# Kernel optimization log

Hardware: AMD Instinct MI355X
Metric: run time of the kernel (lower is better)

The kernel has to match this reference:

```python
import jax, jax.numpy as jnp
import numpy as np

# Model dims (match init_kwargs)
D_MODEL = 512
NUM_EXPERTS = 8
TOP_K = 2
FFN_MULT = 2
HIDDEN = FFN_MULT * D_MODEL
BATCH, SEQ = 4, 2048


def setup_inputs() -> dict:
    key = jax.random.key(0)
    k_x, k_g, k_bg, k_w1, k_w3, k_w2 = jax.random.split(key, 6)
    sd = 1.0 / np.sqrt(D_MODEL).astype(np.float32)
    sh = 1.0 / np.sqrt(HIDDEN).astype(np.float32)
    return {
        "x": jax.random.normal(k_x, (BATCH, SEQ, D_MODEL), dtype=jnp.float32),
        # gate: nn.Linear(d_model, num_experts) with bias
        "Wg": jax.random.normal(k_g, (D_MODEL, NUM_EXPERTS), dtype=jnp.float32) * sd,
        "bg": jax.random.normal(k_bg, (NUM_EXPERTS,), dtype=jnp.float32) * 0.01,
        # stacked per-expert SwiGLU FFN params (no bias, LLaMA-style)
        "W1": jax.random.normal(k_w1, (NUM_EXPERTS, D_MODEL, HIDDEN), dtype=jnp.float32) * sd,
        "W3": jax.random.normal(k_w3, (NUM_EXPERTS, D_MODEL, HIDDEN), dtype=jnp.float32) * sd,
        "W2": jax.random.normal(k_w2, (NUM_EXPERTS, HIDDEN, D_MODEL), dtype=jnp.float32) * sh,
    }


def reference(x, Wg, bg, W1, W3, W2):
    B, S, D = x.shape
    E = Wg.shape[1]
    xt = x.reshape(-1, D)                        # [T, D], T = B*S
    T = xt.shape[0]

    # Router: top-k over experts, softmax over the k selected logits
    logits = xt @ Wg + bg                        # [T, E]
    top_vals, top_idx = jax.lax.top_k(logits, TOP_K)  # [T, K]
    top_probs = jax.nn.softmax(top_vals, axis=-1)     # [T, K]

    # Dense per-(token, expert) combine weight; zero where expert not selected.
    # top-k indices are distinct per token so scatter-add == scatter-set.
    gate_w = jnp.zeros((T, E), dtype=xt.dtype).at[
        jnp.arange(T)[:, None], top_idx
    ].add(top_probs)                              # [T, E]

    # Loop over experts (fixed, small), accumulate weighted expert outputs.
    def body(y, expert):
        w1, w3, w2, g = expert                   # g: [T]
        h = jax.nn.silu(xt @ w1) * (xt @ w3)     # [T, H]
        return y + g[:, None] * (h @ w2), None

    y0 = jnp.zeros_like(xt)
    y, _ = jax.lax.scan(body, y0, (W1, W3, W2, gate_w.T))
    return y.reshape(B, S, D)
```

## Files before the change

kernel.cpp:

```cpp
#include <hip/hip_runtime.h>
#include <hip/hip_bf16.h>

#define TOKENS 8192
#define DM 512
#define NE 8
#define HID 1024
#define NSLOT (TOKENS * 2)
#define NB 32

#define BM 128
#define BN 64
#define BK 64
#define MAXTILE 136

typedef __bf16 bf16x8 __attribute__((ext_vector_type(8)));
typedef float floatx4 __attribute__((ext_vector_type(4)));
typedef unsigned short u16x8 __attribute__((ext_vector_type(8)));

__device__ __forceinline__ unsigned short f2bf(float f) {
    union { float f; unsigned u; } c; c.f = f;
    unsigned u = c.u;
    u += 0x7fffu + ((u >> 16) & 1u);
    return (unsigned short)(u >> 16);
}

__device__ __forceinline__ void load16_lds(const void* g, void* l) {
    __builtin_amdgcn_global_load_lds(
        (const __attribute__((address_space(1))) unsigned int*)g,
        (__attribute__((address_space(3))) unsigned int*)l, 16, 0, 0);
}

__global__ void cvt_transpose_kernel(const float* __restrict__ W1, const float* __restrict__ W3,
                                     const float* __restrict__ W2,
                                     unsigned short* __restrict__ w1t, unsigned short* __restrict__ w3t,
                                     unsigned short* __restrict__ w2t) {
    __shared__ float tile[64][65];
    const float* src; unsigned short* dst; int K, N;
    if (blockIdx.y == 0)      { src = W1; dst = w1t; K = DM;  N = HID; }
    else if (blockIdx.y == 1) { src = W3; dst = w3t; K = DM;  N = HID; }
    else                      { src = W2; dst = w2t; K = HID; N = DM;  }
    const int tkn = (K >> 6) * (N >> 6);
    int b = blockIdx.x;
    int e = b / tkn;
    int rem = b % tkn;
    const int tn6 = N >> 6;
    int kt = rem / tn6, nt = rem % tn6;
    int tx = threadIdx.x & 15, ty = threadIdx.x >> 4;
    const float* s = src + ((size_t)(e * K + kt * 64 + ty)) * N + nt * 64 + tx * 4;
    #pragma unroll
    for (int i = 0; i < 4; i++) {
        float4 v = *(const float4*)(s + (size_t)(i * 16) * N);
        float* tr = &tile[ty + i * 16][tx * 4];
        tr[0] = v.x; tr[1] = v.y; tr[2] = v.z; tr[3] = v.w;
    }
    __syncthreads();
    int n = threadIdx.x >> 3;
    int c8 = (threadIdx.x & 7) * 8;
    unsigned short* d = dst + ((size_t)(e * N + nt * 64)) * K + kt * 64;
    #pragma unroll
    for (int i = 0; i < 2; i++) {
        int nn = n + i * 32;
        u16x8 r;
        #pragma unroll
        for (int kk = 0; kk < 8; kk++) r[kk] = f2bf(tile[c8 + kk][nn]);
        *(u16x8*)(d + (size_t)nn * K + c8) = r;
    }
}

__global__ void router_kernel(const float* __restrict__ x, const float* __restrict__ Wg,
                              const float* __restrict__ bg,
                              int* __restrict__ top_idx, float* __restrict__ top_p,
                              unsigned short* __restrict__ xb) {
    int lane = threadIdx.x & 63, wave = threadIdx.x >> 6;
    int t = blockIdx.x * 4 + wave;
    const float4* xr4 = (const float4*)(x + (size_t)t * DM) + lane * 2;
    float4 va = xr4[0], vb = xr4[1];
    float xv[8] = {va.x, va.y, va.z, va.w, vb.x, vb.y, vb.z, vb.w};
    u16x8 r;
    #pragma unroll
    for (int j = 0; j < 8; j++) r[j] = f2bf(xv[j]);
    *((u16x8*)(xb + (size_t)t * DM) + lane) = r;

    float acc[NE];
    #pragma unroll
    for (int e = 0; e < NE; e++) acc[e] = 0.f;
    #pragma unroll
    for (int j = 0; j < 8; j++) {
        int d = lane * 8 + j;
        const float4* wr = (const float4*)(Wg + (size_t)d * NE);
        float4 w0 = wr[0], w1 = wr[1];
        float xvj = xv[j];
        acc[0] += xvj * w0.x; acc[1] += xvj * w0.y; acc[2] += xvj * w0.z; acc[3] += xvj * w0.w;
        acc[4] += xvj * w1.x; acc[5] += xvj * w1.y; acc[6] += xvj * w1.z; acc[7] += xvj * w1.w;
    }
    #pragma unroll
    for (int e = 0; e < NE; e++) {
        float v = acc[e];
        #pragma unroll
        for (int off = 32; off > 0; off >>= 1) v += __shfl_down(v, off, 64);
        acc[e] = v;
    }
    if (lane == 0) {
        float best = -1e30f, second = -1e30f;
        int bi = 0, si = 0;
        #pragma unroll
        for (int e = 0; e < NE; e++) {
            float v = acc[e] + bg[e];
            if (v > best) { second = best; si = bi; best = v; bi = e; }
            else if (v > second) { second = v; si = e; }
        }
        float ex = __expf(second - best);
        float inv = 1.f / (1.f + ex);
        top_idx[t * 2] = bi;  top_idx[t * 2 + 1] = si;
        top_p[t * 2] = inv;   top_p[t * 2 + 1] = ex * inv;
    }
}

__global__ void hist_kernel(const int* __restrict__ top_idx, int* __restrict__ block_hist) {
    __shared__ int h[NE];
    int b = blockIdx.x, tid = threadIdx.x;
    if (tid < NE) h[tid] = 0;
    __syncthreads();
    int t = b * 256 + tid;
    atomicAdd(&h[top_idx[t * 2]], 1);
    atomicAdd(&h[top_idx[t * 2 + 1]], 1);
    __syncthreads();
    if (tid < NE) block_hist[b * NE + tid] = h[tid];
}

__global__ void build_kernel(const int* __restrict__ top_idx, const float* __restrict__ top_p,
                             const int* __restrict__ block_hist,
                             int* __restrict__ rows, float* __restrict__ gates,
                             int* __restrict__ slot_of,
                             int* __restrict__ counts, int* __restrict__ offsets) {
    __shared__ int hist_s[NB * NE];
    __shared__ int tot_s[NE];
    __shared__ int offs_s[NE];
    __shared__ int cur[NE];
    int b = blockIdx.x, tid = threadIdx.x;
    if (tid < NB * NE) hist_s[tid] = block_hist[tid];
    __syncthreads();
    int mybase = 0;
    if (tid < NE) {
        int run = 0;
        for (int bb = 0; bb < NB; bb++) {
            if (bb == b) mybase = run;
            run += hist_s[bb * NE + tid];
        }
        tot_s[tid] = run;
    }
    __syncthreads();
    if (tid == 0) {
        int s = 0;
        for (int e = 0; e < NE; e++) { offs_s[e] = s; s += tot_s[e]; }
    }
    __syncthreads();
    if (tid < NE) {
        cur[tid] = offs_s[tid] + mybase;
        if (b == 0) { counts[tid] = tot_s[tid]; offsets[tid] = offs_s[tid]; }
    }
    __syncthreads();
    int t = b * 256 + tid;
    #pragma unroll
    for (int k = 0; k < 2; k++) {
        int e = top_idx[t * 2 + k];
        int slot = atomicAdd(&cur[e], 1);
        rows[slot] = t;
        gates[slot] = top_p[t * 2 + k];
        slot_of[t * 2 + k] = slot;
    }
}

__device__ __forceinline__ bool tile_lookup(const int* counts, const int* offsets, int gy,
                                            int& e, int& mt, int& cnt, int& off) {
    int bacc = 0;
    #pragma unroll
    for (int ee = 0; ee < NE; ee++) {
        int c = counts[ee];
        int ntl = (c + BM - 1) >> 7;
        if (gy < bacc + ntl) { e = ee; mt = gy - bacc; cnt = c; off = offsets[ee]; return true; }
        bacc += ntl;
    }
    return false;
}

__global__ __launch_bounds__(256) void gemm1_kernel(
    const unsigned short* __restrict__ xb,
    const unsigned short* __restrict__ w1t,
    const unsigned short* __restrict__ w3t,
    unsigned short* __restrict__ Hb,
    const int* __restrict__ rows, const int* __restrict__ counts,
    const int* __restrict__ offsets) {
    const int lid = blockIdx.x;
    const int xcd = lid & 7;
    const int j = lid >> 3;
    const int gy = xcd * (MAXTILE / 8) + (j >> 4);
    const int nt = j & 15;
    int e, mt, cnt, off;
    if (!tile_lookup(counts, offsets, gy, e, mt, cnt, off)) return;

    __shared__ unsigned short As[2][BM * BK];
    __shared__ unsigned short B1s[2][BN * BK];
    __shared__ unsigned short B3s[2][BN * BK];

    const int tid = threadIdx.x;
    const int lane = tid & 63, wave = tid >> 6;
    const int lrow8 = lane >> 3;
    const int lchunk = (lane & 7) ^ lrow8;

    const unsigned short* a_g[4];
    #pragma unroll
    for (int i = 0; i < 4; i++) {
        int r = (wave * 4 + i) * 8 + lrow8;
        int gr = mt * BM + r;
        int tok = rows[off + (gr < cnt ? gr : 0)];
        a_g[i] = xb + (size_t)tok * DM + lchunk * 8;
    }
    const unsigned short* b1_g[2]; const unsigned short* b3_g[2];
    #pragma unroll
    for (int i = 0; i < 2; i++) {
        int r = (wave * 2 + i) * 8 + lrow8;
        b1_g[i] = w1t + ((size_t)e * HID + nt * BN + r) * DM + lchunk * 8;
        b3_g[i] = w3t + ((size_t)e * HID + nt * BN + r) * DM + lchunk * 8;
    }

    const int l15 = lane & 15, quad = lane >> 4;
    const int sw = l15 & 7;

    floatx4 acc1[2][4], acc3[2][4];
    #pragma unroll
    for (int i = 0; i < 2; i++)
        #pragma unroll
        for (int j2 = 0; j2 < 4; j2++) {
            acc1[i][j2] = (floatx4){0.f, 0.f, 0.f, 0.f};
            acc3[i][j2] = (floatx4){0.f, 0.f, 0.f, 0.f};
        }

    auto stage = [&](int k0, int b) {
        #pragma unroll
        for (int i = 0; i < 4; i++) load16_lds(a_g[i] + k0, &As[b][(wave * 4 + i) * 512]);
        #pragma unroll
        for (int i = 0; i < 2; i++) {
            load16_lds(b1_g[i] + k0, &B1s[b][(wave * 2 + i) * 512]);
            load16_lds(b3_g[i] + k0, &B3s[b][(wave * 2 + i) * 512]);
        }
    };
    auto compute = [&](int b) {
        #pragma unroll
        for (int kk = 0; kk < 2; kk++) {
            const int qc = kk * 4 + quad;
            const int ch = (qc ^ sw) << 3;
            bf16x8 af[2], b1f[4], b3f[4];
            #pragma unroll
            for (int mi = 0; mi < 2; mi++)
                af[mi] = *(const bf16x8*)(&As[b][(wave * 32 + mi * 16 + l15) * 64 + ch]);
            #pragma unroll
            for (int ni = 0; ni < 4; ni++) {
                b1f[ni] = *(const bf16x8*)(&B1s[b][(ni * 16 + l15) * 64 + ch]);
                b3f[ni] = *(const bf16x8*)(&B3s[b][(ni * 16 + l15) * 64 + ch]);
            }
            #pragma unroll
            for (int mi = 0; mi < 2; mi++)
                #pragma unroll
                for (int ni = 0; ni < 4; ni++) {
                    acc1[mi][ni] = __builtin_amdgcn_mfma_f32_16x16x32_bf16(af[mi], b1f[ni], acc1[mi][ni], 0, 0, 0);
                    acc3[mi][ni] = __builtin_amdgcn_mfma_f32_16x16x32_bf16(af[mi], b3f[ni], acc3[mi][ni], 0, 0, 0);
                }
        }
    };

    const int NI = DM / BK;
    stage(0, 0);
    #pragma unroll
    for (int i = 0; i < NI; i += 2) {
        __syncthreads();
        if (i + 1 < NI) stage((i + 1) * BK, 1);
        compute(0);
        __syncthreads();
        if (i + 2 < NI) stage((i + 2) * BK, 0);
        compute(1);
    }
    #pragma unroll
    for (int mi = 0; mi < 2; mi++) {
        #pragma unroll
        for (int r = 0; r < 4; r++) {
            int mloc = wave * 32 + mi * 16 + quad * 4 + r;
            int gi = mt * BM + mloc;
            if (gi < cnt) {
                size_t rowbase = (size_t)(off + gi) * HID + nt * BN;
                #pragma unroll
                for (int ni = 0; ni < 4; ni++) {
                    float z1 = acc1[mi][ni][r];
                    float z3 = acc3[mi][ni][r];
                    float h = (z1 / (1.f + __expf(-z1))) * z3;
                    Hb[rowbase + ni * 16 + l15] = f2bf(h);
                }
            }
        }
    }
}

__global__ __launch_bounds__(256) void gemm2_kernel(
    const unsigned short* __restrict__ Hb,
    const unsigned short* __restrict__ w2t,
    unsigned short* __restrict__ P,
    const float* __restrict__ gates,
    const int* __restrict__ counts, const int* __restrict__ offsets) {
    const int lid = blockIdx.x;
    const int xcd = lid & 7;
    const int j = lid >> 3;
    const int gy = xcd * (MAXTILE / 8) + (j >> 3);
    const int nt = j & 7;
    int e, mt, cnt, off;
    if (!tile_lookup(counts, offsets, gy, e, mt, cnt, off)) return;

    __shared__ unsigned short As[2][BM * BK];
    __shared__ unsigned short Bs[2][BN * BK];

    const int tid = threadIdx.x;
    const int lane = tid & 63, wave = tid >> 6;
    const int lrow8 = lane >> 3;
    const int lchunk = (lane & 7) ^ lrow8;

    const unsigned short* a_g[4];
    #pragma unroll
    for (int i = 0; i < 4; i++) {
        int r = (wave * 4 + i) * 8 + lrow8;
        int sl = off + mt * BM + r;
        if (sl >= NSLOT) sl = NSLOT - 1;
        a_g[i] = Hb + (size_t)sl * HID + lchunk * 8;
    }
    const unsigned short* b_g[2];
    #pragma unroll
    for (int i = 0; i < 2; i++) {
        int r = (wave * 2 + i) * 8 + lrow8;
        b_g[i] = w2t + ((size_t)e * DM + nt * BN + r) * HID + lchunk * 8;
    }

    const int l15 = lane & 15, quad = lane >> 4;
    const int sw = l15 & 7;

    floatx4 acc[2][4];
    #pragma unroll
    for (int i = 0; i < 2; i++)
        #pragma unroll
        for (int j2 = 0; j2 < 4; j2++) acc[i][j2] = (floatx4){0.f, 0.f, 0.f, 0.f};

    auto stage = [&](int k0, int b) {
        #pragma unroll
        for (int i = 0; i < 4; i++) load16_lds(a_g[i] + k0, &As[b][(wave * 4 + i) * 512]);
        #pragma unroll
        for (int i = 0; i < 2; i++) load16_lds(b_g[i] + k0, &Bs[b][(wave * 2 + i) * 512]);
    };
    auto compute = [&](int b) {
        #pragma unroll
        for (int kk = 0; kk < 2; kk++) {
            const int qc = kk * 4 + quad;
            const int ch = (qc ^ sw) << 3;
            bf16x8 af[2], bf[4];
            #pragma unroll
            for (int mi = 0; mi < 2; mi++)
                af[mi] = *(const bf16x8*)(&As[b][(wave * 32 + mi * 16 + l15) * 64 + ch]);
            #pragma unroll
            for (int ni = 0; ni < 4; ni++)
                bf[ni] = *(const bf16x8*)(&Bs[b][(ni * 16 + l15) * 64 + ch]);
            #pragma unroll
            for (int mi = 0; mi < 2; mi++)
                #pragma unroll
                for (int ni = 0; ni < 4; ni++)
                    acc[mi][ni] = __builtin_amdgcn_mfma_f32_16x16x32_bf16(af[mi], bf[ni], acc[mi][ni], 0, 0, 0);
        }
    };

    const int NI = HID / BK;
    stage(0, 0);
    #pragma unroll
    for (int i = 0; i < NI; i += 2) {
        __syncthreads();
        if (i + 1 < NI) stage((i + 1) * BK, 1);
        compute(0);
        __syncthreads();
        if (i + 2 < NI) stage((i + 2) * BK, 0);
        compute(1);
    }
    #pragma unroll
    for (int mi = 0; mi < 2; mi++) {
        #pragma unroll
        for (int r = 0; r < 4; r++) {
            int mloc = wave * 32 + mi * 16 + quad * 4 + r;
            int gi = mt * BM + mloc;
            if (gi < cnt) {
                int slot = off + gi;
                float g = gates[slot];
                #pragma unroll
                for (int ni = 0; ni < 4; ni++) {
                    int col = nt * BN + ni * 16 + l15;
                    P[(size_t)slot * DM + col] = f2bf(g * acc[mi][ni][r]);
                }
            }
        }
    }
}

__global__ void combine_kernel(const unsigned short* __restrict__ P,
                               const int* __restrict__ slot_of, float* __restrict__ y) {
    int i = blockIdx.x * blockDim.x + threadIdx.x;
    int t = i / (DM / 8);
    int c8 = i % (DM / 8);
    int s0 = slot_of[t * 2], s1 = slot_of[t * 2 + 1];
    uint4 a = *(const uint4*)(P + (size_t)s0 * DM + c8 * 8);
    uint4 b = *(const uint4*)(P + (size_t)s1 * DM + c8 * 8);
    float o[8];
    const unsigned* aw = (const unsigned*)&a;
    const unsigned* bw = (const unsigned*)&b;
    #pragma unroll
    for (int j = 0; j < 4; j++) {
        union { unsigned u; float f; } al, ah, bl, bh;
        al.u = aw[j] << 16; ah.u = aw[j] & 0xffff0000u;
        bl.u = bw[j] << 16; bh.u = bw[j] & 0xffff0000u;
        o[j * 2]     = al.f + bl.f;
        o[j * 2 + 1] = ah.f + bh.f;
    }
    float4* yo = (float4*)(y + (size_t)t * DM + c8 * 8);
    yo[0] = make_float4(o[0], o[1], o[2], o[3]);
    yo[1] = make_float4(o[4], o[5], o[6], o[7]);
}

extern "C" void kernel_launch(void* const* d_in, const int* in_sizes, int n_in,
                              void* d_out, int out_size, void* d_ws, size_t ws_size,
                              hipStream_t stream) {
    (void)in_sizes; (void)n_in; (void)out_size; (void)ws_size;
    const float* x  = (const float*)d_in[0];
    const float* Wg = (const float*)d_in[1];
    const float* bg = (const float*)d_in[2];
    const float* W1 = (const float*)d_in[3];
    const float* W3 = (const float*)d_in[4];
    const float* W2 = (const float*)d_in[5];
    float* y = (float*)d_out;

    char* p = (char*)d_ws;
    auto carve = [&](size_t bytes) -> char* {
        char* r = p;
        p += (bytes + 255) & ~(size_t)255;
        return r;
    };
    unsigned short* xb   = (unsigned short*)carve((size_t)TOKENS * DM * 2);
    unsigned short* w1t  = (unsigned short*)carve((size_t)NE * DM * HID * 2);
    unsigned short* w3t  = (unsigned short*)carve((size_t)NE * DM * HID * 2);
    unsigned short* w2t  = (unsigned short*)carve((size_t)NE * HID * DM * 2);
    unsigned short* Hb   = (unsigned short*)carve((size_t)NSLOT * HID * 2);
    int*   rows    = (int*)carve(NSLOT * 4);
    float* gates   = (float*)carve(NSLOT * 4);
    int*   slot_of = (int*)carve(NSLOT * 4);
    int*   tidx    = (int*)carve((size_t)TOKENS * 2 * 4);
    float* tp      = (float*)carve((size_t)TOKENS * 2 * 4);
    int*   counts  = (int*)carve(256);
    int*   offsets = (int*)carve(256);
    int*   bhist   = (int*)carve((size_t)NB * NE * 4);
    unsigned short* P = w1t;

    router_kernel<<<dim3(TOKENS / 4), dim3(256), 0, stream>>>(x, Wg, bg, tidx, tp, xb);
    cvt_transpose_kernel<<<dim3(NE * 8 * 16, 3), dim3(256), 0, stream>>>(W1, W3, W2, w1t, w3t, w2t);
    hist_kernel<<<dim3(NB), dim3(256), 0, stream>>>(tidx, bhist);
    build_kernel<<<dim3(NB), dim3(256), 0, stream>>>(tidx, tp, bhist, rows, gates, slot_of, counts, offsets);
    gemm1_kernel<<<dim3((HID / BN) * MAXTILE), dim3(256), 0, stream>>>(xb, w1t, w3t, Hb, rows, counts, offsets);
    gemm2_kernel<<<dim3((DM / BN) * MAXTILE), dim3(256), 0, stream>>>(Hb, w2t, P, gates, counts, offsets);
    combine_kernel<<<dim3((TOKENS * DM / 8) / 256), dim3(256), 0, stream>>>(P, slot_of, y);
}
```

Baseline: 225.1 us.

## Merge router and weight-convert kernels; use 2x2 wave tiling in expert GEMMs

The router and weight convert/transpose kernels are combined into one launch, with block index ranges selecting the role, which removes a launch and lets the two independent jobs run side by side. In both expert GEMMs, the four waves now cover 64x32 sub-tiles arranged 2x2 instead of 32x64 strips. Each wave reads half as much B fragment data from LDS per k-step while doing the same number of MFMAs. The merged kernel reserves the 64x65 float LDS tile in router blocks too, which may reduce their occupancy.

Measured after the change: 228.8 us. No clear change (+1.6%).

```diff
diff --git a/kernel.cpp b/kernel.cpp
--- a/kernel.cpp
+++ b/kernel.cpp
@@ -30,89 +30,93 @@
         (__attribute__((address_space(3))) unsigned int*)l, 16, 0, 0);
 }
 
-__global__ void cvt_transpose_kernel(const float* __restrict__ W1, const float* __restrict__ W3,
-                                     const float* __restrict__ W2,
-                                     unsigned short* __restrict__ w1t, unsigned short* __restrict__ w3t,
-                                     unsigned short* __restrict__ w2t) {
+__global__ void prep_kernel(const float* __restrict__ x, const float* __restrict__ Wg,
+                            const float* __restrict__ bg,
+                            int* __restrict__ top_idx, float* __restrict__ top_p,
+                            unsigned short* __restrict__ xb,
+                            const float* __restrict__ W1, const float* __restrict__ W3,
+                            const float* __restrict__ W2,
+                            unsigned short* __restrict__ w1t, unsigned short* __restrict__ w3t,
+                            unsigned short* __restrict__ w2t) {
     __shared__ float tile[64][65];
-    const float* src; unsigned short* dst; int K, N;
-    if (blockIdx.y == 0)      { src = W1; dst = w1t; K = DM;  N = HID; }
-    else if (blockIdx.y == 1) { src = W3; dst = w3t; K = DM;  N = HID; }
-    else                      { src = W2; dst = w2t; K = HID; N = DM;  }
-    const int tkn = (K >> 6) * (N >> 6);
-    int b = blockIdx.x;
-    int e = b / tkn;
-    int rem = b % tkn;
-    const int tn6 = N >> 6;
-    int kt = rem / tn6, nt = rem % tn6;
-    int tx = threadIdx.x & 15, ty = threadIdx.x >> 4;
-    const float* s = src + ((size_t)(e * K + kt * 64 + ty)) * N + nt * 64 + tx * 4;
-    #pragma unroll
-    for (int i = 0; i < 4; i++) {
-        float4 v = *(const float4*)(s + (size_t)(i * 16) * N);
-        float* tr = &tile[ty + i * 16][tx * 4];
-        tr[0] = v.x; tr[1] = v.y; tr[2] = v.z; tr[3] = v.w;
-    }
-    __syncthreads();
-    int n = threadIdx.x >> 3;
-    int c8 = (threadIdx.x & 7) * 8;
-    unsigned short* d = dst + ((size_t)(e * N + nt * 64)) * K + kt * 64;
-    #pragma unroll
-    for (int i = 0; i < 2; i++) {
-        int nn = n + i * 32;
+    const int blk = blockIdx.x;
+    if (blk < TOKENS / 4) {
+        int lane = threadIdx.x & 63, wave = threadIdx.x >> 6;
+        int t = blk * 4 + wave;
+        const float4* xr4 = (const float4*)(x + (size_t)t * DM) + lane * 2;
+        float4 va = xr4[0], vb = xr4[1];
+        float xv[8] = {va.x, va.y, va.z, va.w, vb.x, vb.y, vb.z, vb.w};
         u16x8 r;
         #pragma unroll
-        for (int kk = 0; kk < 8; kk++) r[kk] = f2bf(tile[c8 + kk][nn]);
-        *(u16x8*)(d + (size_t)nn * K + c8) = r;
-    }
-}
-
-__global__ void router_kernel(const float* __restrict__ x, const float* __restrict__ Wg,
-                              const float* __restrict__ bg,
-                              int* __restrict__ top_idx, float* __restrict__ top_p,
-                              unsigned short* __restrict__ xb) {
-    int lane = threadIdx.x & 63, wave = threadIdx.x >> 6;
-    int t = blockIdx.x * 4 + wave;
-    const float4* xr4 = (const float4*)(x + (size_t)t * DM) + lane * 2;
-    float4 va = xr4[0], vb = xr4[1];
-    float xv[8] = {va.x, va.y, va.z, va.w, vb.x, vb.y, vb.z, vb.w};
-    u16x8 r;
-    #pragma unroll
-    for (int j = 0; j < 8; j++) r[j] = f2bf(xv[j]);
-    *((u16x8*)(xb + (size_t)t * DM) + lane) = r;
-
-    float acc[NE];
-    #pragma unroll
-    for (int e = 0; e < NE; e++) acc[e] = 0.f;
-    #pragma unroll
-    for (int j = 0; j < 8; j++) {
-        int d = lane * 8 + j;
-        const float4* wr = (const float4*)(Wg + (size_t)d * NE);
-        float4 w0 = wr[0], w1 = wr[1];
-        float xvj = xv[j];
-        acc[0] += xvj * w0.x; acc[1] += xvj * w0.y; acc[2] += xvj * w0.z; acc[3] += xvj * w0.w;
-        acc[4] += xvj * w1.x; acc[5] += xvj * w1.y; acc[6] += xvj * w1.z; acc[7] += xvj * w1.w;
-    }
-    #pragma unroll
-    for (int e = 0; e < NE; e++) {
-        float v = acc[e];
-        #pragma unroll
-        for (int off = 32; off > 0; off >>= 1) v += __shfl_down(v, off, 64);
-        acc[e] = v;
-    }
-    if (lane == 0) {
-        float best = -1e30f, second = -1e30f;
-        int bi = 0, si = 0;
+        for (int j = 0; j < 8; j++) r[j] = f2bf(xv[j]);
+        *((u16x8*)(xb + (size_t)t * DM) + lane) = r;
+
+        float acc[NE];
+        #pragma unroll
+        for (int e = 0; e < NE; e++) acc[e] = 0.f;
+        #pragma unroll
+        for (int j = 0; j < 8; j++) {
+            int d = lane * 8 + j;
+            const float4* wr = (const float4*)(Wg + (size_t)d * NE);
+            float4 w0 = wr[0], w1 = wr[1];
+            float xvj = xv[j];
+            acc[0] += xvj * w0.x; acc[1] += xvj * w0.y; acc[2] += xvj * w0.z; acc[3] += xvj * w0.w;
+            acc[4] += xvj * w1.x; acc[5] += xvj * w1.y; acc[6] += xvj * w1.z; acc[7] += xvj * w1.w;
+        }
         #pragma unroll
         for (int e = 0; e < NE; e++) {
-            float v = acc[e] + bg[e];
-            if (v > best) { second = best; si = bi; best = v; bi = e; }
-            else if (v > second) { second = v; si = e; }
-        }
-        float ex = __expf(second - best);
-        float inv = 1.f / (1.f + ex);
-        top_idx[t * 2] = bi;  top_idx[t * 2 + 1] = si;
-        top_p[t * 2] = inv;   top_p[t * 2 + 1] = ex * inv;
+            float v = acc[e];
+            #pragma unroll
+            for (int off = 32; off > 0; off >>= 1) v += __shfl_down(v, off, 64);
+            acc[e] = v;
+        }
+        if (lane == 0) {
+            float best = -1e30f, second = -1e30f;
+            int bi = 0, si = 0;
+            #pragma unroll
+            for (int e = 0; e < NE; e++) {
+                float v = acc[e] + bg[e];
+                if (v > best) { second = best; si = bi; best = v; bi = e; }
+                else if (v > second) { second = v; si = e; }
+            }
+            float ex = __expf(second - best);
+            float inv = 1.f / (1.f + ex);
+            top_idx[t * 2] = bi;  top_idx[t * 2 + 1] = si;
+            top_p[t * 2] = inv;   top_p[t * 2 + 1] = ex * inv;
+        }
+    } else {
+        int bb = blk - TOKENS / 4;
+        int widx = bb >> 10;
+        int b = bb & 1023;
+        const float* src; unsigned short* dst; int K, N;
+        if (widx == 0)      { src = W1; dst = w1t; K = DM;  N = HID; }
+        else if (widx == 1) { src = W3; dst = w3t; K = DM;  N = HID; }
+        else                { src = W2; dst = w2t; K = HID; N = DM;  }
+        const int tkn = (K >> 6) * (N >> 6);
+        int e = b / tkn;
+        int rem = b % tkn;
+        const int tn6 = N >> 6;
+        int kt = rem / tn6, nt = rem % tn6;
+        int tx = threadIdx.x & 15, ty = threadIdx.x >> 4;
+        const float* s = src + ((size_t)(e * K + kt * 64 + ty)) * N + nt * 64 + tx * 4;
+        #pragma unroll
+        for (int i = 0; i < 4; i++) {
+            float4 v = *(const float4*)(s + (size_t)(i * 16) * N);
+            float* tr = &tile[ty + i * 16][tx * 4];
+            tr[0] = v.x; tr[1] = v.y; tr[2] = v.z; tr[3] = v.w;
+        }
+        __syncthreads();
+        int n = threadIdx.x >> 3;
+        int c8 = (threadIdx.x & 7) * 8;
+        unsigned short* d = dst + ((size_t)(e * N + nt * 64)) * K + kt * 64;
+        #pragma unroll
+        for (int i = 0; i < 2; i++) {
+            int nn = n + i * 32;
+            u16x8 rr;
+            #pragma unroll
+            for (int kk = 0; kk < 8; kk++) rr[kk] = f2bf(tile[c8 + kk][nn]);
+            *(u16x8*)(d + (size_t)nn * K + c8) = rr;
+        }
     }
 }
 
@@ -226,12 +230,14 @@
 
     const int l15 = lane & 15, quad = lane >> 4;
     const int sw = l15 & 7;
-
-    floatx4 acc1[2][4], acc3[2][4];
-    #pragma unroll
-    for (int i = 0; i < 2; i++)
-        #pragma unroll
-        for (int j2 = 0; j2 < 4; j2++) {
+    const int m0 = (wave >> 1) * 64;
+    const int n0 = (wave & 1) * 32;
+
+    floatx4 acc1[4][2], acc3[4][2];
+    #pragma unroll
+    for (int i = 0; i < 4; i++)
+        #pragma unroll
+        for (int j2 = 0; j2 < 2; j2++) {
             acc1[i][j2] = (floatx4){0.f, 0.f, 0.f, 0.f};
             acc3[i][j2] = (floatx4){0.f, 0.f, 0.f, 0.f};
         }
@@ -250,19 +256,19 @@
         for (int kk = 0; kk < 2; kk++) {
             const int qc = kk * 4 + quad;
             const int ch = (qc ^ sw) << 3;
-            bf16x8 af[2], b1f[4], b3f[4];
-            #pragma unroll
-            for (int mi = 0; mi < 2; mi++)
-                af[mi] = *(const bf16x8*)(&As[b][(wave * 32 + mi * 16 + l15) * 64 + ch]);
-            #pragma unroll
-            for (int ni = 0; ni < 4; ni++) {
-                b1f[ni] = *(const bf16x8*)(&B1s[b][(ni * 16 + l15) * 64 + ch]);
-                b3f[ni] = *(const bf16x8*)(&B3s[b][(ni * 16 + l15) * 64 + ch]);
+            bf16x8 af[4], b1f[2], b3f[2];
+            #pragma unroll
+            for (int mi = 0; mi < 4; mi++)
+                af[mi] = *(const bf16x8*)(&As[b][(m0 + mi * 16 + l15) * 64 + ch]);
+            #pragma unroll
+            for (int ni = 0; ni < 2; ni++) {
+                b1f[ni] = *(const bf16x8*)(&B1s[b][(n0 + ni * 16 + l15) * 64 + ch]);
+                b3f[ni] = *(const bf16x8*)(&B3s[b][(n0 + ni * 16 + l15) * 64 + ch]);
             }
             #pragma unroll
-            for (int mi = 0; mi < 2; mi++)
+            for (int mi = 0; mi < 4; mi++)
                 #pragma unroll
-                for (int ni = 0; ni < 4; ni++) {
+                for (int ni = 0; ni < 2; ni++) {
                     acc1[mi][ni] = __builtin_amdgcn_mfma_f32_16x16x32_bf16(af[mi], b1f[ni], acc1[mi][ni], 0, 0, 0);
                     acc3[mi][ni] = __builtin_amdgcn_mfma_f32_16x16x32_bf16(af[mi], b3f[ni], acc3[mi][ni], 0, 0, 0);
                 }
@@ -281,15 +287,15 @@
         compute(1);
     }
     #pragma unroll
-    for (int mi = 0; mi < 2; mi++) {
+    for (int mi = 0; mi < 4; mi++) {
         #pragma unroll
         for (int r = 0; r < 4; r++) {
-            int mloc = wave * 32 + mi * 16 + quad * 4 + r;
+            int mloc = m0 + mi * 16 + quad * 4 + r;
             int gi = mt * BM + mloc;
             if (gi < cnt) {
-                size_t rowbase = (size_t)(off + gi) * HID + nt * BN;
+                size_t rowbase = (size_t)(off + gi) * HID + nt * BN + n0;
                 #pragma unroll
-                for (int ni = 0; ni < 4; ni++) {
+                for (int ni = 0; ni < 2; ni++) {
                     float z1 = acc1[mi][ni][r];
                     float z3 = acc3[mi][ni][r];
                     float h = (z1 / (1.f + __expf(-z1))) * z3;
@@ -339,12 +345,14 @@
 
     const int l15 = lane & 15, quad = lane >> 4;
     const int sw = l15 & 7;
-
-    floatx4 acc[2][4];
-    #pragma unroll
-    for (int i = 0; i < 2; i++)
-        #pragma unroll
-        for (int j2 = 0; j2 < 4; j2++) acc[i][j2] = (floatx4){0.f, 0.f, 0.f, 0.f};
+    const int m0 = (wave >> 1) * 64;
+    const int n0 = (wave & 1) * 32;
+
+    floatx4 acc[4][2];
+    #pragma unroll
+    for (int i = 0; i < 4; i++)
+        #pragma unroll
+        for (int j2 = 0; j2 < 2; j2++) acc[i][j2] = (floatx4){0.f, 0.f, 0.f, 0.f};
 
     auto stage = [&](int k0, int b) {
         #pragma unroll
@@ -357,17 +365,17 @@
         for (int kk = 0; kk < 2; kk++) {
             const int qc = kk * 4 + quad;
             const int ch = (qc ^ sw) << 3;
-            bf16x8 af[2], bf[4];
-            #pragma unroll
-            for (int mi = 0; mi < 2; mi++)
-                af[mi] = *(const bf16x8*)(&As[b][(wave * 32 + mi * 16 + l15) * 64 + ch]);
-            #pragma unroll
-            for (int ni = 0; ni < 4; ni++)
-                bf[ni] = *(const bf16x8*)(&Bs[b][(ni * 16 + l15) * 64 + ch]);
-            #pragma unroll
-            for (int mi = 0; mi < 2; mi++)
+            bf16x8 af[4], bf[2];
+            #pragma unroll
+            for (int mi = 0; mi < 4; mi++)
+                af[mi] = *(const bf16x8*)(&As[b][(m0 + mi * 16 + l15) * 64 + ch]);
+            #pragma unroll
+            for (int ni = 0; ni < 2; ni++)
+                bf[ni] = *(const bf16x8*)(&Bs[b][(n0 + ni * 16 + l15) * 64 + ch]);
+            #pragma unroll
+            for (int mi = 0; mi < 4; mi++)
                 #pragma unroll
-                for (int ni = 0; ni < 4; ni++)
+                for (int ni = 0; ni < 2; ni++)
                     acc[mi][ni] = __builtin_amdgcn_mfma_f32_16x16x32_bf16(af[mi], bf[ni], acc[mi][ni], 0, 0, 0);
         }
     };
@@ -384,17 +392,17 @@
         compute(1);
     }
     #pragma unroll
-    for (int mi = 0; mi < 2; mi++) {
+    for (int mi = 0; mi < 4; mi++) {
         #pragma unroll
         for (int r = 0; r < 4; r++) {
-            int mloc = wave * 32 + mi * 16 + quad * 4 + r;
+            int mloc = m0 + mi * 16 + quad * 4 + r;
             int gi = mt * BM + mloc;
             if (gi < cnt) {
                 int slot = off + gi;
                 float g = gates[slot];
                 #pragma unroll
-                for (int ni = 0; ni < 4; ni++) {
-                    int col = nt * BN + ni * 16 + l15;
+                for (int ni = 0; ni < 2; ni++) {
+                    int col = nt * BN + n0 + ni * 16 + l15;
                     P[(size_t)slot * DM + col] = f2bf(g * acc[mi][ni][r]);
                 }
             }
@@ -459,8 +467,8 @@
     int*   bhist   = (int*)carve((size_t)NB * NE * 4);
     unsigned short* P = w1t;
 
-    router_kernel<<<dim3(TOKENS / 4), dim3(256), 0, stream>>>(x, Wg, bg, tidx, tp, xb);
-    cvt_transpose_kernel<<<dim3(NE * 8 * 16, 3), dim3(256), 0, stream>>>(W1, W3, W2, w1t, w3t, w2t);
+    prep_kernel<<<dim3(TOKENS / 4 + 3 * 1024), dim3(256), 0, stream>>>(
+        x, Wg, bg, tidx, tp, xb, W1, W3, W2, w1t, w3t, w2t);
     hist_kernel<<<dim3(NB), dim3(256), 0, stream>>>(tidx, bhist);
     build_kernel<<<dim3(NB), dim3(256), 0, stream>>>(tidx, tp, bhist, rows, gates, slot_of, counts, offsets);
     gemm1_kernel<<<dim3((HID / BN) * MAXTILE), dim3(256), 0, stream>>>(xb, w1t, w3t, Hb, rows, counts, offsets);
```
